# Kernel tuning notes

Hardware: AMD Instinct MI355X
Metric: run time of the kernel (lower is better)

The kernel has to match this reference:

```python
import jax, jax.numpy as jnp
import numpy as np

COS_EPS = 1e-8  # torch.nn.CosineSimilarity default eps
B, L, D = 32, 512, 1024
S, E = 256, 64
POS = 17


def _padded_idxs(key, batch, max_len, seq_len, min_frac=0.5):
    """Random first-subword indices in [1, seq_len) with trailing zero padding."""
    k1, k2 = jax.random.split(key)
    lens = jax.random.randint(k1, (batch,), int(max_len * min_frac), max_len + 1)
    vals = jax.random.randint(k2, (batch, max_len), 1, seq_len)
    col = jnp.arange(max_len)[None, :]
    return jnp.where(col < lens[:, None], vals, 0).astype(jnp.int32)


def setup_inputs() -> dict:
    key = jax.random.key(0)
    ks = jax.random.split(key, 7)
    all_embeddings = jax.random.normal(ks[0], (B, L, D), dtype=jnp.float32)
    W = jax.random.uniform(ks[1], (D, D), dtype=jnp.float32) / np.sqrt(D)
    lin_w = jax.random.normal(ks[2], (2, 2 * D + POS), dtype=jnp.float32) * 0.02
    lin_b = jnp.zeros((2,), dtype=jnp.float32)
    idxs_to_collect_sent = _padded_idxs(ks[3], B, S, L)
    idxs_to_collect_event = _padded_idxs(ks[4], B, E, L)
    pos_tag = jax.random.randint(ks[5], (B, S), -1, POS - 1).astype(jnp.int32)
    return {
        "all_embeddings": all_embeddings,
        "W": W,
        "lin_w": lin_w,
        "lin_b": lin_b,
        "idxs_to_collect_sent": idxs_to_collect_sent,
        "idxs_to_collect_event": idxs_to_collect_event,
        "pos_tag": pos_tag,
    }


def _gather_pad(all_embeddings, idxs):
    # idxs has valid (>0) entries at the front, zeros as trailing pad, so the
    # per-sample compact-gather-then-pad loop is equivalent to gather + mask.
    mask = (idxs > 0)  # [B, T]
    gathered = jnp.take_along_axis(
        all_embeddings, jnp.maximum(idxs, 0)[..., None], axis=1)  # [B, T, D]
    return gathered * mask[..., None].astype(all_embeddings.dtype), mask


def reference(all_embeddings, W, lin_w, lin_b,
              idxs_to_collect_sent, idxs_to_collect_event, pos_tag):
    sent, _ = _gather_pad(all_embeddings, idxs_to_collect_sent)       # [B,S,D]
    event, ev_mask = _gather_pad(all_embeddings, idxs_to_collect_event)  # [B,E,D]

    # map_numerator = 1 / number of valid event tokens per sample
    map_num = 1.0 / jnp.sum(ev_mask, axis=-1).astype(sent.dtype)  # [B]

    # cosine similarity between (sent @ W) and event embeddings
    a = jnp.einsum('bsd,de->bse', sent, W)                 # [B,S,D]
    num = jnp.einsum('bsd,bed->bse', a, event)             # [B,S,E]
    na = jnp.maximum(jnp.linalg.norm(a, axis=-1), COS_EPS)       # [B,S]
    ne = jnp.maximum(jnp.linalg.norm(event, axis=-1), COS_EPS)   # [B,E]
    logits = num / (na[:, :, None] * ne[:, None, :])       # [B,S,E]

    sent2event_att = jnp.einsum('bse,bed->bsd', logits, event) * map_num[:, None, None]

    pos = jnp.where(pos_tag < 0, POS - 1, pos_tag)
    pos_oh = jax.nn.one_hot(pos, POS, dtype=sent.dtype)    # [B,S,17]

    feat = jnp.concatenate([sent, sent2event_att, pos_oh], axis=-1)  # [B,S,2D+17]
    return feat @ lin_w.T + lin_b                           # [B,S,2]
```

## Files before the change

kernel.cpp:

```cpp
#include <hip/hip_runtime.h>

#define B_ 32
#define L_ 512
#define D_ 1024
#define S_ 256
#define E_ 64
#define POS_ 17
#define LWS 2065
#define M_ (B_*S_)

typedef __attribute__((ext_vector_type(8))) short short8v;
typedef __attribute__((ext_vector_type(4))) float f32x4;
typedef __attribute__((ext_vector_type(16))) float f32x16;
typedef __attribute__((ext_vector_type(4))) unsigned short us4;

__device__ __forceinline__ unsigned short f2bf(float x) {
  union { float f; unsigned u; } v; v.f = x;
  unsigned r = v.u + 0x7FFFu + ((v.u >> 16) & 1u);
  return (unsigned short)(r >> 16);
}
__device__ __forceinline__ float bf2f(unsigned short b) {
  union { unsigned u; float f; } v; v.u = ((unsigned)b) << 16;
  return v.f;
}
__device__ __forceinline__ void async16(void* lds, const void* g) {
  __builtin_amdgcn_global_load_lds(
      (const __attribute__((address_space(1))) unsigned int*)(unsigned long long)g,
      (__attribute__((address_space(3))) unsigned int*)(unsigned int)(unsigned long long)lds,
      16, 0, 0);
}

#define VMCNT8 asm volatile("s_waitcnt vmcnt(8)" ::: "memory")
#define VMCNT0 asm volatile("s_waitcnt vmcnt(0)" ::: "memory")
#define BARRIER __builtin_amdgcn_s_barrier()

__global__ __launch_bounds__(256) void prep_all(
    const float* __restrict__ emb, const float* __restrict__ W,
    const float* __restrict__ lin_w, const float* __restrict__ lin_b,
    const int* __restrict__ idx_s, const int* __restrict__ idx_e,
    const int* __restrict__ pos_tag,
    unsigned short* __restrict__ sentb, unsigned short* __restrict__ evb,
    unsigned short* __restrict__ Wt,
    float* __restrict__ base, float* __restrict__ ne, float* __restrict__ evw) {
  int bid = blockIdx.x;
  int t = threadIdx.x;

  if (bid >= 2560) {
    __shared__ float tile[32][33];
    int tt = bid - 2560;
    int bx = tt & 31, by = tt >> 5;
    int tx = t & 31, ty = t >> 5;
#pragma unroll
    for (int i = 0; i < 4; i++)
      tile[ty + i * 8][tx] = W[(size_t)(by * 32 + ty + i * 8) * D_ + bx * 32 + tx];
    __syncthreads();
#pragma unroll
    for (int i = 0; i < 4; i++)
      Wt[(size_t)(bx * 32 + ty + i * 8) * D_ + by * 32 + tx] = f2bf(tile[tx][ty + i * 8]);
    return;
  }

  int lane = t & 63, w = t >> 6;
  bool is_sent = bid < 2048;
  int row = is_sent ? (((bid & 7) << 10) | ((bid >> 3) << 2) | w)
                    : (((bid - 2048) << 2) | w);
  int b = is_sent ? (row >> 8) : (row >> 6);
  int idx = is_sent ? idx_s[row] : idx_e[row];
  float msk = idx > 0 ? 1.0f : 0.0f;
  const float* src = emb + ((size_t)b * L_ + (idx > 0 ? idx : 0)) * D_;

  float r0 = 0.f, r1 = 0.f, sq = 0.f;
  const float* lw0 = is_sent ? lin_w : (lin_w + D_);
  const float* lw1 = is_sent ? (lin_w + LWS) : (lin_w + LWS + D_);
  unsigned short* dst = is_sent ? (sentb + (size_t)row * D_)
                                : (evb + (size_t)row * D_);
#pragma unroll
  for (int j = 0; j < 4; j++) {
    int d = j * 256 + lane * 4;
    float4 v = *(const float4*)(src + d);
    v.x *= msk; v.y *= msk; v.z *= msk; v.w *= msk;
    us4 o; o.x = f2bf(v.x); o.y = f2bf(v.y); o.z = f2bf(v.z); o.w = f2bf(v.w);
    *(us4*)&dst[d] = o;
    float4 c0 = *(const float4*)(lw0 + d);
    r0 += v.x * c0.x + v.y * c0.y + v.z * c0.z + v.w * c0.w;
    r1 += v.x * lw1[d] + v.y * lw1[d + 1] + v.z * lw1[d + 2] + v.w * lw1[d + 3];
    if (!is_sent) sq += v.x * v.x + v.y * v.y + v.z * v.z + v.w * v.w;
  }
#pragma unroll
  for (int off = 32; off; off >>= 1) {
    r0 += __shfl_xor(r0, off);
    r1 += __shfl_xor(r1, off);
  }
  if (is_sent) {
    if (lane == 0) {
      int p = pos_tag[row]; if (p < 0) p = POS_ - 1;
      base[(size_t)row * 2 + 0] = r0 + lin_b[0] + lin_w[2 * D_ + p];
      base[(size_t)row * 2 + 1] = r1 + lin_b[1] + lin_w[LWS + 2 * D_ + p];
    }
  } else {
#pragma unroll
    for (int off = 32; off; off >>= 1) sq += __shfl_xor(sq, off);
    if (lane == 0) {
      ne[row] = fmaxf(sqrtf(sq), 1e-8f);
      evw[(size_t)row * 2 + 0] = r0;
      evw[(size_t)row * 2 + 1] = r1;
    }
  }
}

__device__ __forceinline__ void stage_g(const char* gA, const char* gB,
    unsigned short* bA, unsigned short* bB, int t, int kt) {
  int sc = ((t & 7) ^ ((t >> 3) & 7)) << 4;
#pragma unroll
  for (int i = 0; i < 4; i++) {
    int row = i * 32 + (t >> 3);
    size_t src = (size_t)row * (D_ * 2) + (size_t)kt * 128 + sc;
    async16((char*)bA + i * 4096 + t * 16, gA + src);
    async16((char*)bB + i * 4096 + t * 16, gB + src);
  }
}
__device__ __forceinline__ void comp_g(const unsigned short* bA,
    const unsigned short* bB, f32x16 (&acc)[2][2], int wr, int wc, int fr32, int hi1) {
  int x = fr32 & 7;
#pragma unroll
  for (int ks = 0; ks < 4; ks++) {
    int co = ((ks * 2 + hi1) ^ x) << 3;
    short8v a[2], bv[2];
#pragma unroll
    for (int m = 0; m < 2; m++)
      a[m] = *(const short8v*)&bA[(wr * 64 + m * 32 + fr32) * 64 + co];
#pragma unroll
    for (int n = 0; n < 2; n++)
      bv[n] = *(const short8v*)&bB[(wc * 64 + n * 32 + fr32) * 64 + co];
#pragma unroll
    for (int m = 0; m < 2; m++)
#pragma unroll
      for (int n = 0; n < 2; n++)
        acc[m][n] = __builtin_amdgcn_mfma_f32_32x32x16_bf16(a[m], bv[n], acc[m][n], 0, 0, 0);
  }
}

__global__ __launch_bounds__(256) void gemm_aw(
    const unsigned short* __restrict__ A,
    const unsigned short* __restrict__ Bt,
    unsigned short* __restrict__ C) {
  const int K = D_, N = D_;
  __shared__ unsigned short sA0[128 * 64], sA1[128 * 64];
  __shared__ unsigned short sB0[128 * 64], sB1[128 * 64];
  int t = threadIdx.x;
  int w = t >> 6, lane = t & 63;
  int wr = w >> 1, wc = w & 1;
  int fr32 = lane & 31, hi1 = lane >> 5;
  int bid = blockIdx.x;
  int wg = ((bid & 7) << 6) | (bid >> 3);
  int n0 = (wg & 7) * 128, m0 = (wg >> 3) * 128;
  f32x16 acc[2][2];
#pragma unroll
  for (int m = 0; m < 2; m++)
#pragma unroll
    for (int n = 0; n < 2; n++)
#pragma unroll
      for (int r = 0; r < 16; r++) acc[m][n][r] = 0.f;

  const char* gA = (const char*)(A + (size_t)m0 * K);
  const char* gB = (const char*)(Bt + (size_t)n0 * K);

  stage_g(gA, gB, sA0, sB0, t, 0);
#pragma unroll 1
  for (int kt = 0; kt < 14; kt += 2) {
    stage_g(gA, gB, sA1, sB1, t, kt + 1);
    VMCNT8; BARRIER;
    __builtin_amdgcn_sched_barrier(0);
    comp_g(sA0, sB0, acc, wr, wc, fr32, hi1);
    BARRIER;
    stage_g(gA, gB, sA0, sB0, t, kt + 2);
    VMCNT8; BARRIER;
    __builtin_amdgcn_sched_barrier(0);
    comp_g(sA1, sB1, acc, wr, wc, fr32, hi1);
    BARRIER;
  }
  stage_g(gA, gB, sA1, sB1, t, 15);
  VMCNT8; BARRIER;
  __builtin_amdgcn_sched_barrier(0);
  comp_g(sA0, sB0, acc, wr, wc, fr32, hi1);
  VMCNT0; BARRIER;
  __builtin_amdgcn_sched_barrier(0);
  comp_g(sA1, sB1, acc, wr, wc, fr32, hi1);

#pragma unroll
  for (int m = 0; m < 2; m++) {
#pragma unroll
    for (int n = 0; n < 2; n++) {
#pragma unroll
      for (int r = 0; r < 16; r++) {
        int crow = (r & 3) + 8 * (r >> 2) + 4 * hi1;
        int row = wr * 64 + m * 32 + crow;
        C[(size_t)(m0 + row) * N + n0 + wc * 64 + n * 32 + fr32] = f2bf(acc[m][n][r]);
      }
    }
  }
}

__device__ __forceinline__ void stage_a(const char* gA, const char* gE,
    unsigned short* bA, unsigned short* bE, int t, int kt) {
#pragma unroll
  for (int i = 0; i < 2; i++) {
    int idx = i * 256 + t;
    int row = idx >> 4;
    int ch = (idx & 15) ^ (row & 15);
    async16((char*)bA + idx * 16, gA + (size_t)row * (D_ * 2) + (size_t)kt * 256 + ch * 16);
  }
#pragma unroll
  for (int i = 0; i < 4; i++) {
    int idx = i * 256 + t;
    int row = idx >> 4;
    int ch = (idx & 15) ^ (row & 15);
    async16((char*)bE + idx * 16, gE + (size_t)row * (D_ * 2) + (size_t)kt * 256 + ch * 16);
  }
}
__device__ __forceinline__ void comp_a(const unsigned short* bA,
    const unsigned short* bE, f32x4 (&acc)[2], float& rsq, int w, int fr, int hi) {
  int rowA = (w >> 1) * 16 + fr;
  int ch = w & 1;
#pragma unroll
  for (int ks = 0; ks < 4; ks++) {
    int ca = ((ks * 4 + hi) ^ (rowA & 15)) << 3;
    short8v af = *(const short8v*)&bA[rowA * 128 + ca];
    if (ch == 0) {
#pragma unroll
      for (int j = 0; j < 8; j++) { float xv = bf2f((unsigned short)af[j]); rsq += xv * xv; }
    }
#pragma unroll
    for (int n = 0; n < 2; n++) {
      int rowE = ch * 32 + n * 16 + fr;
      int ce = ((ks * 4 + hi) ^ (rowE & 15)) << 3;
      short8v bv = *(const short8v*)&bE[rowE * 128 + ce];
      acc[n] = __builtin_amdgcn_mfma_f32_16x16x32_bf16(af, bv, acc[n], 0, 0, 0);
    }
  }
}

__global__ __launch_bounds__(256) void attn_ep(
    const unsigned short* __restrict__ Abf,
    const unsigned short* __restrict__ Ebf,
    const int* __restrict__ idx_e,
    const float* __restrict__ ne, const float* __restrict__ evw,
    const float* __restrict__ base,
    float* __restrict__ out) {
  int bid = blockIdx.x;
  int xcd = bid & 7, loc = bid >> 3;
  int b = xcd * 4 + (loc >> 3);
  int s0 = (loc & 7) * 32;
  __shared__ unsigned short sA0[32 * 128], sA1[32 * 128];
  __shared__ unsigned short sE0[64 * 128], sE1[64 * 128];
  __shared__ float sRne[E_], sEvw[E_][2], sRna[32], sP[2][32][2];
  __shared__ float sMapn;
  int t = threadIdx.x;
  int w = t >> 6, lane = t & 63;
  int fr = lane & 15, hi = lane >> 4;
  if (t < E_) {
    sRne[t] = 1.0f / ne[b * E_ + t];
    sEvw[t][0] = evw[(size_t)(b * E_ + t) * 2 + 0];
    sEvw[t][1] = evw[(size_t)(b * E_ + t) * 2 + 1];
    unsigned long long mball = __ballot(idx_e[b * E_ + t] > 0);
    if (t == 0) sMapn = 1.0f / (float)__popcll(mball);
  }
  f32x4 acc[2];
#pragma unroll
  for (int n = 0; n < 2; n++) acc[n] = f32x4{0.f, 0.f, 0.f, 0.f};
  float rsq = 0.f;

  const char* gA = (const char*)(Abf + ((size_t)b * S_ + s0) * D_);
  const char* gE = (const char*)(Ebf + (size_t)b * E_ * D_);

  stage_a(gA, gE, sA0, sE0, t, 0);
  __syncthreads();
#pragma unroll 1
  for (int kt = 0; kt < 8; kt += 2) {
    stage_a(gA, gE, sA1, sE1, t, kt + 1);
    comp_a(sA0, sE0, acc, rsq, w, fr, hi);
    __syncthreads();
    if (kt + 2 < 8) stage_a(gA, gE, sA0, sE0, t, kt + 2);
    comp_a(sA1, sE1, acc, rsq, w, fr, hi);
    __syncthreads();
  }
  rsq += __shfl_xor(rsq, 16);
  rsq += __shfl_xor(rsq, 32);
  if ((w & 1) == 0 && lane < 16)
    sRna[(w >> 1) * 16 + lane] = 1.0f / fmaxf(sqrtf(rsq), 1e-8f);
  __syncthreads();

  int ch = w & 1;
#pragma unroll
  for (int r = 0; r < 4; r++) {
    int srl = (w >> 1) * 16 + hi * 4 + r;
    float rna = sRna[srl];
    float a0 = 0.f, a1 = 0.f;
#pragma unroll
    for (int n = 0; n < 2; n++) {
      int e = ch * 32 + n * 16 + fr;
      float lg = acc[n][r] * rna * sRne[e];
      a0 += lg * sEvw[e][0];
      a1 += lg * sEvw[e][1];
    }
#pragma unroll
    for (int off = 1; off < 16; off <<= 1) {
      a0 += __shfl_xor(a0, off);
      a1 += __shfl_xor(a1, off);
    }
    if (fr == 0) { sP[ch][srl][0] = a0; sP[ch][srl][1] = a1; }
  }
  __syncthreads();
  if (t < 64) {
    int row = t >> 1, c = t & 1;
    float v = sP[0][row][c] + sP[1][row][c];
    size_t sg = (size_t)b * S_ + s0 + row;
    out[sg * 2 + c] = base[sg * 2 + c] + sMapn * v;
  }
}

extern "C" void kernel_launch(void* const* d_in, const int* in_sizes, int n_in,
                              void* d_out, int out_size, void* d_ws, size_t ws_size,
                              hipStream_t stream) {
  const float* emb   = (const float*)d_in[0];
  const float* W     = (const float*)d_in[1];
  const float* lin_w = (const float*)d_in[2];
  const float* lin_b = (const float*)d_in[3];
  const int* idx_s   = (const int*)d_in[4];
  const int* idx_e   = (const int*)d_in[5];
  const int* pos     = (const int*)d_in[6];
  float* out = (float*)d_out;

  char* ws = (char*)d_ws;
  const size_t MB = 1024 * 1024;
  unsigned short* sentb = (unsigned short*)(ws);
  unsigned short* abf   = (unsigned short*)(ws + 16 * MB);
  unsigned short* evb   = (unsigned short*)(ws + 32 * MB);
  unsigned short* Wt    = (unsigned short*)(ws + 36 * MB);
  float* ne   = (float*)(ws + 38 * MB);
  float* evw  = ne + 2048;
  float* base = evw + 4096;

  prep_all<<<3584, 256, 0, stream>>>(
      emb, W, lin_w, lin_b, idx_s, idx_e, pos, sentb, evb, Wt, base, ne, evw);
  gemm_aw<<<512, 256, 0, stream>>>(sentb, Wt, abf);
  attn_ep<<<B_ * 8, 256, 0, stream>>>(abf, evb, idx_e, ne, evw, base, out);
}
```

Before: 43.40 us.

## Load GEMM B operands directly from global into registers instead of LDS

In both the W GEMM and the attention kernel, the B/event operand is no longer staged through LDS with async copies. Each wave now loads its MFMA B fragments straight from global memory, and the vmcnt wait is lowered to match the halved async load count. The goal is to cut LDS footprint and staging traffic, raising occupancy. The cost is that B loads become exposed global latency inside the compute loop, and the global reads may be less coalesced. The prep kernel also vectorizes the second lin_w row read into a float4.

```diff
diff --git a/kernel.cpp b/kernel.cpp
--- a/kernel.cpp
+++ b/kernel.cpp
@@ -30,7 +30,7 @@
       16, 0, 0);
 }
 
-#define VMCNT8 asm volatile("s_waitcnt vmcnt(8)" ::: "memory")
+#define VMCNT4 asm volatile("s_waitcnt vmcnt(4)" ::: "memory")
 #define VMCNT0 asm volatile("s_waitcnt vmcnt(0)" ::: "memory")
 #define BARRIER __builtin_amdgcn_s_barrier()
 
@@ -82,8 +82,9 @@
     us4 o; o.x = f2bf(v.x); o.y = f2bf(v.y); o.z = f2bf(v.z); o.w = f2bf(v.w);
     *(us4*)&dst[d] = o;
     float4 c0 = *(const float4*)(lw0 + d);
+    float4 c1 = *(const float4*)(lw1 + d);
     r0 += v.x * c0.x + v.y * c0.y + v.z * c0.z + v.w * c0.w;
-    r1 += v.x * lw1[d] + v.y * lw1[d + 1] + v.z * lw1[d + 2] + v.w * lw1[d + 3];
+    r1 += v.x * c1.x + v.y * c1.y + v.z * c1.z + v.w * c1.w;
     if (!is_sent) sq += v.x * v.x + v.y * v.y + v.z * v.z + v.w * v.w;
   }
 #pragma unroll
@@ -108,30 +109,31 @@
   }
 }
 
-__device__ __forceinline__ void stage_g(const char* gA, const char* gB,
-    unsigned short* bA, unsigned short* bB, int t, int kt) {
+__device__ __forceinline__ void stage_g(const char* gA, unsigned short* bA,
+                                        int t, int kt) {
   int sc = ((t & 7) ^ ((t >> 3) & 7)) << 4;
 #pragma unroll
   for (int i = 0; i < 4; i++) {
     int row = i * 32 + (t >> 3);
     size_t src = (size_t)row * (D_ * 2) + (size_t)kt * 128 + sc;
     async16((char*)bA + i * 4096 + t * 16, gA + src);
-    async16((char*)bB + i * 4096 + t * 16, gB + src);
   }
 }
 __device__ __forceinline__ void comp_g(const unsigned short* bA,
-    const unsigned short* bB, f32x16 (&acc)[2][2], int wr, int wc, int fr32, int hi1) {
+    const unsigned short* gB, int kt, f32x16 (&acc)[2][2],
+    int wr, int fr32, int hi1) {
   int x = fr32 & 7;
 #pragma unroll
   for (int ks = 0; ks < 4; ks++) {
     int co = ((ks * 2 + hi1) ^ x) << 3;
     short8v a[2], bv[2];
 #pragma unroll
+    for (int n = 0; n < 2; n++)
+      bv[n] = *(const short8v*)&gB[(size_t)(n * 32 + fr32) * D_ +
+                                   kt * 64 + ks * 16 + hi1 * 8];
+#pragma unroll
     for (int m = 0; m < 2; m++)
       a[m] = *(const short8v*)&bA[(wr * 64 + m * 32 + fr32) * 64 + co];
-#pragma unroll
-    for (int n = 0; n < 2; n++)
-      bv[n] = *(const short8v*)&bB[(wc * 64 + n * 32 + fr32) * 64 + co];
 #pragma unroll
     for (int m = 0; m < 2; m++)
 #pragma unroll
@@ -146,7 +148,6 @@
     unsigned short* __restrict__ C) {
   const int K = D_, N = D_;
   __shared__ unsigned short sA0[128 * 64], sA1[128 * 64];
-  __shared__ unsigned short sB0[128 * 64], sB1[128 * 64];
   int t = threadIdx.x;
   int w = t >> 6, lane = t & 63;
   int wr = w >> 1, wc = w & 1;
@@ -163,29 +164,29 @@
       for (int r = 0; r < 16; r++) acc[m][n][r] = 0.f;
 
   const char* gA = (const char*)(A + (size_t)m0 * K);
-  const char* gB = (const char*)(Bt + (size_t)n0 * K);
-
-  stage_g(gA, gB, sA0, sB0, t, 0);
+  const unsigned short* gB = Bt + (size_t)(n0 + wc * 64) * K;
+
+  stage_g(gA, sA0, t, 0);
 #pragma unroll 1
   for (int kt = 0; kt < 14; kt += 2) {
-    stage_g(gA, gB, sA1, sB1, t, kt + 1);
-    VMCNT8; BARRIER;
+    stage_g(gA, sA1, t, kt + 1);
+    VMCNT4; BARRIER;
     __builtin_amdgcn_sched_barrier(0);
-    comp_g(sA0, sB0, acc, wr, wc, fr32, hi1);
+    comp_g(sA0, gB, kt, acc, wr, fr32, hi1);
     BARRIER;
-    stage_g(gA, gB, sA0, sB0, t, kt + 2);
-    VMCNT8; BARRIER;
+    stage_g(gA, sA0, t, kt + 2);
+    VMCNT4; BARRIER;
     __builtin_amdgcn_sched_barrier(0);
-    comp_g(sA1, sB1, acc, wr, wc, fr32, hi1);
+    comp_g(sA1, gB, kt + 1, acc, wr, fr32, hi1);
     BARRIER;
   }
-  stage_g(gA, gB, sA1, sB1, t, 15);
-  VMCNT8; BARRIER;
+  stage_g(gA, sA1, t, 15);
+  VMCNT4; BARRIER;
   __builtin_amdgcn_sched_barrier(0);
-  comp_g(sA0, sB0, acc, wr, wc, fr32, hi1);
+  comp_g(sA0, gB, 14, acc, wr, fr32, hi1);
   VMCNT0; BARRIER;
   __builtin_amdgcn_sched_barrier(0);
-  comp_g(sA1, sB1, acc, wr, wc, fr32, hi1);
+  comp_g(sA1, gB, 15, acc, wr, fr32, hi1);
 
 #pragma unroll
   for (int m = 0; m < 2; m++) {
@@ -201,8 +202,8 @@
   }
 }
 
-__device__ __forceinline__ void stage_a(const char* gA, const char* gE,
-    unsigned short* bA, unsigned short* bE, int t, int kt) {
+__device__ __forceinline__ void stage_a(const char* gA, unsigned short* bA,
+                                        int t, int kt) {
 #pragma unroll
   for (int i = 0; i < 2; i++) {
     int idx = i * 256 + t;
@@ -210,16 +211,10 @@
     int ch = (idx & 15) ^ (row & 15);
     async16((char*)bA + idx * 16, gA + (size_t)row * (D_ * 2) + (size_t)kt * 256 + ch * 16);
   }
-#pragma unroll
-  for (int i = 0; i < 4; i++) {
-    int idx = i * 256 + t;
-    int row = idx >> 4;
-    int ch = (idx & 15) ^ (row & 15);
-    async16((char*)bE + idx * 16, gE + (size_t)row * (D_ * 2) + (size_t)kt * 256 + ch * 16);
-  }
 }
 __device__ __forceinline__ void comp_a(const unsigned short* bA,
-    const unsigned short* bE, f32x4 (&acc)[2], float& rsq, int w, int fr, int hi) {
+    const unsigned short* gE, int kt, f32x4 (&acc)[2], float& rsq,
+    int w, int fr, int hi) {
   int rowA = (w >> 1) * 16 + fr;
   int ch = w & 1;
 #pragma unroll
@@ -233,8 +228,8 @@
 #pragma unroll
     for (int n = 0; n < 2; n++) {
       int rowE = ch * 32 + n * 16 + fr;
-      int ce = ((ks * 4 + hi) ^ (rowE & 15)) << 3;
-      short8v bv = *(const short8v*)&bE[rowE * 128 + ce];
+      short8v bv = *(const short8v*)&gE[(size_t)rowE * D_ +
+                                        kt * 128 + ks * 32 + hi * 8];
       acc[n] = __builtin_amdgcn_mfma_f32_16x16x32_bf16(af, bv, acc[n], 0, 0, 0);
     }
   }
@@ -252,7 +247,6 @@
   int b = xcd * 4 + (loc >> 3);
   int s0 = (loc & 7) * 32;
   __shared__ unsigned short sA0[32 * 128], sA1[32 * 128];
-  __shared__ unsigned short sE0[64 * 128], sE1[64 * 128];
   __shared__ float sRne[E_], sEvw[E_][2], sRna[32], sP[2][32][2];
   __shared__ float sMapn;
   int t = threadIdx.x;
@@ -271,17 +265,17 @@
   float rsq = 0.f;
 
   const char* gA = (const char*)(Abf + ((size_t)b * S_ + s0) * D_);
-  const char* gE = (const char*)(Ebf + (size_t)b * E_ * D_);
-
-  stage_a(gA, gE, sA0, sE0, t, 0);
+  const unsigned short* gE = Ebf + (size_t)b * E_ * D_;
+
+  stage_a(gA, sA0, t, 0);
   __syncthreads();
 #pragma unroll 1
   for (int kt = 0; kt < 8; kt += 2) {
-    stage_a(gA, gE, sA1, sE1, t, kt + 1);
-    comp_a(sA0, sE0, acc, rsq, w, fr, hi);
+    stage_a(gA, sA1, t, kt + 1);
+    comp_a(sA0, gE, kt, acc, rsq, w, fr, hi);
     __syncthreads();
-    if (kt + 2 < 8) stage_a(gA, gE, sA0, sE0, t, kt + 2);
-    comp_a(sA1, sE1, acc, rsq, w, fr, hi);
+    if (kt + 2 < 8) stage_a(gA, sA0, t, kt + 2);
+    comp_a(sA1, gE, kt + 1, acc, rsq, w, fr, hi);
     __syncthreads();
   }
   rsq += __shfl_xor(rsq, 16);
```

Result: slower. 68.11 us (+56.9%).
